# Optimization experiments

Hardware: AMD Instinct MI355X
Metric: run time of the kernel (lower is better)

The kernel has to match this reference:

```python
import jax, jax.numpy as jnp
import numpy as np

# Static config (Swin-T stage 1, SW-MSA)
B = 32; H = 56; W = 56; C = 96; NH = 3; WS = 7; SHIFT = 3
N = WS * WS                 # tokens per window (49)
NW = (H // WS) * (W // WS)  # windows per image (64)
HD = C // NH                # head dim (32)
SCALE = HD ** -0.5
EPS = 1e-3  # keras LayerNormalization default epsilon


def _rel_index():
    # Matches tf.stack(tf.meshgrid(h, w)) with default 'xy' indexing
    xx, yy = np.meshgrid(np.arange(WS), np.arange(WS))
    coords = np.stack([xx, yy]).reshape(2, -1)              # [2, 49]
    rel = (coords[:, :, None] - coords[:, None, :]).transpose(1, 2, 0)
    rel[:, :, 0] += WS - 1
    rel[:, :, 1] += WS - 1
    rel[:, :, 0] *= 2 * WS - 1
    return rel.sum(-1)                                       # [49, 49]

REL_IDX = jnp.asarray(_rel_index())


def _attn_mask():
    # Standard Swin shifted-window attention mask
    img = np.zeros((H, W))
    cnt = 0
    sl = (slice(0, -WS), slice(-WS, -SHIFT), slice(-SHIFT, None))
    for hs in sl:
        for ws_ in sl:
            img[hs, ws_] = cnt
            cnt += 1
    win = img.reshape(H // WS, WS, W // WS, WS).transpose(0, 2, 1, 3).reshape(-1, N)
    diff = win[:, None, :] - win[:, :, None]
    return jnp.asarray(np.where(diff != 0, -100.0, 0.0), dtype=np.float32)  # [nW,49,49]

MASK = _attn_mask()


def _ln(x, g, b):
    mu = x.mean(-1, keepdims=True)
    var = ((x - mu) ** 2).mean(-1, keepdims=True)
    return (x - mu) / jnp.sqrt(var + EPS) * g + b


def setup_inputs() -> dict:
    key = jax.random.key(0)
    ks = jax.random.split(key, 6)
    f32 = jnp.float32
    return {
        "x": jax.random.normal(ks[0], (B, H * W, C), f32),
        "norm1_g": jnp.ones((C,), f32), "norm1_b": jnp.zeros((C,), f32),
        "qkv_w": jax.random.normal(ks[1], (C, 3 * C), f32) * 0.02,
        "qkv_b": jnp.zeros((3 * C,), f32),
        "bias_table": jax.random.normal(ks[2], ((2 * WS - 1) ** 2, NH), f32) * 0.02,
        "proj_w": jax.random.normal(ks[3], (C, C), f32) * 0.02,
        "proj_b": jnp.zeros((C,), f32),
        "norm2_g": jnp.ones((C,), f32), "norm2_b": jnp.zeros((C,), f32),
        "fc1_w": jax.random.normal(ks[4], (C, 4 * C), f32) * 0.02,
        "fc1_b": jnp.zeros((4 * C,), f32),
        "fc2_w": jax.random.normal(ks[5], (4 * C, C), f32) * 0.02,
        "fc2_b": jnp.zeros((C,), f32),
    }


def reference(x, norm1_g, norm1_b, qkv_w, qkv_b, bias_table, proj_w, proj_b,
              norm2_g, norm2_b, fc1_w, fc1_b, fc2_w, fc2_b):
    shortcut = x
    h = _ln(x, norm1_g, norm1_b).reshape(B, H, W, C)
    # cyclic shift (SW-MSA)
    h = jnp.roll(h, (-SHIFT, -SHIFT), axis=(1, 2))
    # window partition -> [B*nW, N, C]
    h = h.reshape(B, H // WS, WS, W // WS, WS, C).transpose(0, 1, 3, 2, 4, 5).reshape(-1, N, C)
    qkv = (h @ qkv_w + qkv_b).reshape(-1, N, 3, NH, HD).transpose(2, 0, 3, 1, 4)
    q, k, v = qkv[0], qkv[1], qkv[2]            # each [B*nW, NH, N, HD]
    attn = jnp.einsum('bhnd,bhmd->bhnm', q * SCALE, k)
    bias = bias_table[REL_IDX.reshape(-1)].reshape(N, N, NH).transpose(2, 0, 1)
    attn = attn + bias[None]
    attn = attn.reshape(B, NW, NH, N, N) + MASK[None, :, None]
    attn = attn.reshape(-1, NH, N, N)
    # NOTE: source applies softmax twice (once in branch, once unconditionally)
    attn = jax.nn.softmax(jax.nn.softmax(attn, axis=-1), axis=-1)
    o = jnp.einsum('bhnm,bhmd->bhnd', attn, v).transpose(0, 2, 1, 3).reshape(-1, N, C)
    o = o @ proj_w + proj_b
    # window reverse + reverse cyclic shift
    o = o.reshape(B, H // WS, W // WS, WS, WS, C).transpose(0, 1, 3, 2, 4, 5).reshape(B, H, W, C)
    o = jnp.roll(o, (SHIFT, SHIFT), axis=(1, 2)).reshape(B, H * W, C)
    x = shortcut + o
    y = _ln(x, norm2_g, norm2_b)
    # NOTE: source Mlp applies gelu in Dense activation AND again in call -> double gelu
    y = jax.nn.gelu(y @ fc1_w + fc1_b, approximate=False)
    y = jax.nn.gelu(y, approximate=False)
    y = y @ fc2_w + fc2_b
    return x + y
```

## Files before the change

### kernel.cpp

```cpp
#include <hip/hip_runtime.h>
#include <math.h>

#define BB   32
#define HH   56
#define WWI  56
#define CC   96
#define NHD  3
#define WSZ  7
#define SHF  3
#define NTK  49
#define NWIN 64
#define HDM  32
#define TOT  (BB*HH*WWI)
#define QKSCALE 0.17677669529663687f
#define LEPS 1e-3f

typedef __attribute__((ext_vector_type(8))) short s8v;
typedef __attribute__((ext_vector_type(4))) float fx4;
typedef unsigned long long ull_t;

#define MFMA16(a,b,c) __builtin_amdgcn_mfma_f32_16x16x32_bf16((a),(b),(c),0,0,0)

__device__ __forceinline__ unsigned short f2bf(float f) {
    union { float f; unsigned u; } v; v.f = f;
    unsigned r = v.u + 0x7FFFu + ((v.u >> 16) & 1u);
    return (unsigned short)(r >> 16);
}

__device__ __forceinline__ float gelu_t(float x) {
    float x3 = x * x * x;
    float z = -1.5957691216f * fmaf(0.044715f, x3, x);
    return x * __builtin_amdgcn_rcpf(1.f + __expf(z));
}

__device__ __forceinline__ int wtok_to_orig(int wt) {
    int win = wt / NTK;
    int p   = wt - win * NTK;
    int b   = win >> 6;
    int w   = win & 63;
    int wi = w >> 3, wj = w & 7;
    int pi = p / WSZ, pj = p - pi * WSZ;
    int r = wi * WSZ + pi + SHF; if (r >= HH) r -= HH;
    int c = wj * WSZ + pj + SHF; if (c >= WWI) c -= WWI;
    return b * (HH * WWI) + r * WWI + c;
}

__device__ __forceinline__ void ln_frag(const float* __restrict__ row,
                                        const float* __restrict__ gg,
                                        const float* __restrict__ bb,
                                        int g4, s8v ha[3])
{
    float h[24];
    #pragma unroll
    for (int ks = 0; ks < 3; ++ks) {
        fx4 v0 = *reinterpret_cast<const fx4*>(row + ks * 32 + g4 * 8);
        fx4 v1 = *reinterpret_cast<const fx4*>(row + ks * 32 + g4 * 8 + 4);
        h[ks*8+0]=v0.x; h[ks*8+1]=v0.y; h[ks*8+2]=v0.z; h[ks*8+3]=v0.w;
        h[ks*8+4]=v1.x; h[ks*8+5]=v1.y; h[ks*8+6]=v1.z; h[ks*8+7]=v1.w;
    }
    float s = 0.f, s2 = 0.f;
    #pragma unroll
    for (int j = 0; j < 24; ++j) { s += h[j]; s2 = fmaf(h[j], h[j], s2); }
    s  += __shfl_xor(s, 16);  s  += __shfl_xor(s, 32);
    s2 += __shfl_xor(s2, 16); s2 += __shfl_xor(s2, 32);
    const float mu = s * (1.f/CC);
    const float rs = rsqrtf(s2 * (1.f/CC) - mu * mu + LEPS);
    #pragma unroll
    for (int ks = 0; ks < 3; ++ks) {
        union { s8v v; unsigned short u[8]; } p;
        #pragma unroll
        for (int j = 0; j < 8; ++j) {
            int c = ks * 32 + g4 * 8 + j;
            p.u[j] = f2bf((h[ks*8+j] - mu) * rs * gg[c] + bb[c]);
        }
        ha[ks] = p.v;
    }
}

extern "C" __global__ void p0_prep(const float* __restrict__ qw, const float* __restrict__ pw,
                                   const float* __restrict__ w1, const float* __restrict__ w2,
                                   const float* __restrict__ btab,
                                   unsigned short* __restrict__ wsw)
{
    int i = blockIdx.x * 256 + threadIdx.x;
    if (i < 27648) {
        int n = i / 96, k = i - n * 96;
        float v = qw[k * 288 + n];
        if (n < 96) v *= QKSCALE;
        wsw[i] = f2bf(v);
    } else if (i < 36864) {
        int j = i - 27648; int n = j / 96, k = j - n * 96;
        wsw[i] = f2bf(pw[k * 96 + n]);
    } else if (i < 73728) {
        int j = i - 36864; int n = j / 96, k = j - n * 96;
        wsw[i] = f2bf(w1[k * 384 + n]);
    } else if (i < 110592) {
        int j = i - 73728; int n = j / 384, k = j - n * 384;
        wsw[i] = f2bf(w2[k * 96 + n]);
    } else if (i < 148224) {
        float* bm = (float*)(wsw + 110592);
        int j = i - 110592;
        int n = j & 63, mh = j >> 6;
        int m = mh % 49, t = mh / 49;
        int hd = t % 3, cls = t / 3;
        float val = 0.f;
        if (n < 49) {
            int it = m / 7, jt = m - it * 7;
            int iu = n / 7, ju = n - iu * 7;
            int li  = (cls & 2) ? (it < 4 ? 1 : 2) : 0;
            int lj  = (cls & 1) ? (jt < 4 ? 1 : 2) : 0;
            int lui = (cls & 2) ? (iu < 4 ? 1 : 2) : 0;
            int luj = (cls & 1) ? (ju < 4 ? 1 : 2) : 0;
            int bidx = (jt - ju + 6) * 13 + (it - iu + 6);
            val = btab[bidx * 3 + hd] + ((li*3+lj) == (lui*3+luj) ? 0.f : -100.f);
        }
        bm[j] = val;
    }
}

#define LDH 104
extern "C" __global__ void __launch_bounds__(512, 4) k1_qkv(
    const float* __restrict__ x, const float* __restrict__ g1, const float* __restrict__ b1,
    const unsigned short* __restrict__ qwt, const float* __restrict__ qb,
    unsigned short* __restrict__ qkvb)
{
    __shared__ unsigned short Wc[96 * LDH];
    const int tid = threadIdx.x, wave = tid >> 6, lane = tid & 63;
    const int l15 = lane & 15, g4 = lane >> 4;
    const int blk = blockIdx.x;

    s8v ha[3];
    {
        const int orig = wtok_to_orig(blk * 128 + wave * 16 + l15);
        ln_frag(x + (size_t)orig * CC, g1, b1, g4, ha);
    }

    for (int ck = 0; ck < 3; ++ck) {
        for (int i = tid; i < 96 * 12; i += 512) {
            int r = i / 12, k0 = (i - r * 12) * 8;
            *reinterpret_cast<s8v*>(&Wc[r * LDH + k0]) =
                *reinterpret_cast<const s8v*>(&qwt[(ck * 96 + r) * 96 + k0]);
        }
        __syncthreads();
        fx4 acc[6];
        #pragma unroll
        for (int nt = 0; nt < 6; ++nt) acc[nt] = (fx4){0.f,0.f,0.f,0.f};
        #pragma unroll
        for (int ks = 0; ks < 3; ++ks) {
            #pragma unroll
            for (int nt = 0; nt < 6; ++nt) {
                s8v b = *reinterpret_cast<const s8v*>(&Wc[(nt*16 + l15)*LDH + ks*32 + g4*8]);
                acc[nt] = MFMA16(ha[ks], b, acc[nt]);
            }
        }
        const int rowb = blk * 128 + wave * 16 + g4 * 4;
        const float qmul = (ck == 0) ? QKSCALE : 1.f;
        #pragma unroll
        for (int nt = 0; nt < 6; ++nt) {
            const int col = ck * 96 + nt * 16 + l15;
            const float qbc = qb[col] * qmul;
            #pragma unroll
            for (int r = 0; r < 4; ++r)
                qkvb[(size_t)(rowb + r) * 288 + col] = f2bf(acc[nt][r] + qbc);
        }
        __syncthreads();
    }
}

extern "C" __global__ void __launch_bounds__(64, 2) k2_attn(
    unsigned short* __restrict__ qkvb, const float* __restrict__ bm)
{
    __shared__ unsigned short P[64][72];
    const int lane = threadIdx.x;
    const int l15 = lane & 15, g4 = lane >> 4;
    const int task = blockIdx.x;
    const int win = task / 3, h = task - win * 3;
    const int g0  = win * NTK;
    const int w   = win & 63;
    const int cls = (((w >> 3) == 7) ? 2 : 0) + (((w & 7) == 7) ? 1 : 0);
    const float* BMh = bm + ((size_t)(cls * 3 + h)) * 49 * 64;

    s8v aq[4], bk[4];
    #pragma unroll
    for (int mt = 0; mt < 4; ++mt) {
        int tok = mt * 16 + l15; if (tok > 48) tok = 48;
        const unsigned short* qp = &qkvb[(size_t)(g0 + tok) * 288 + h * HDM + g4 * 8];
        aq[mt] = *reinterpret_cast<const s8v*>(qp);
        bk[mt] = *reinterpret_cast<const s8v*>(qp + 96);
    }

    fx4 sc[4][4];
    #pragma unroll
    for (int mt = 0; mt < 4; ++mt)
        #pragma unroll
        for (int nt = 0; nt < 4; ++nt)
            sc[mt][nt] = MFMA16(aq[mt], bk[nt], ((fx4){0.f,0.f,0.f,0.f}));

    #pragma unroll
    for (int mt = 0; mt < 4; ++mt) {
        #pragma unroll
        for (int r = 0; r < 4; ++r) {
            const int m = mt * 16 + g4 * 4 + r;
            const int mc = m > 48 ? 48 : m;
            float rs1 = 0.f;
            #pragma unroll
            for (int nt = 0; nt < 4; ++nt) {
                const int n = nt * 16 + l15;
                float s = sc[mt][nt][r] + BMh[mc * 64 + n];
                float e = (n < NTK) ? __expf(s) : 0.f;
                sc[mt][nt][r] = e;
                rs1 += e;
            }
            rs1 += __shfl_xor(rs1, 1); rs1 += __shfl_xor(rs1, 2);
            rs1 += __shfl_xor(rs1, 4); rs1 += __shfl_xor(rs1, 8);
            const float iv1 = 1.f / rs1;
            float rs2 = 0.f;
            #pragma unroll
            for (int nt = 0; nt < 4; ++nt) {
                const int n = nt * 16 + l15;
                float e2 = (n < NTK) ? __expf(sc[mt][nt][r] * iv1) : 0.f;
                sc[mt][nt][r] = e2;
                rs2 += e2;
            }
            rs2 += __shfl_xor(rs2, 1); rs2 += __shfl_xor(rs2, 2);
            rs2 += __shfl_xor(rs2, 4); rs2 += __shfl_xor(rs2, 8);
            const float iv2 = 1.f / rs2;
            #pragma unroll
            for (int nt = 0; nt < 4; ++nt)
                P[m][nt * 16 + l15] = f2bf(sc[mt][nt][r] * iv2);
        }
    }
    __syncthreads();

    fx4 oc[4][2];
    #pragma unroll
    for (int mt = 0; mt < 4; ++mt) { oc[mt][0] = (fx4){0.f,0.f,0.f,0.f}; oc[mt][1] = (fx4){0.f,0.f,0.f,0.f}; }
    #pragma unroll
    for (int ks = 0; ks < 2; ++ks) {
        s8v vb[2];
        #pragma unroll
        for (int nt = 0; nt < 2; ++nt) {
            union { s8v v; unsigned short u[8]; } pv;
            #pragma unroll
            for (int j = 0; j < 8; ++j) {
                int tok = ks * 32 + g4 * 8 + j; if (tok > 48) tok = 48;
                pv.u[j] = qkvb[(size_t)(g0 + tok) * 288 + 192 + h * HDM + nt * 16 + l15];
            }
            vb[nt] = pv.v;
        }
        #pragma unroll
        for (int mt = 0; mt < 4; ++mt) {
            s8v pa = *reinterpret_cast<const s8v*>(&P[mt * 16 + l15][ks * 32 + g4 * 8]);
            oc[mt][0] = MFMA16(pa, vb[0], oc[mt][0]);
            oc[mt][1] = MFMA16(pa, vb[1], oc[mt][1]);
        }
    }
    #pragma unroll
    for (int mt = 0; mt < 4; ++mt) {
        #pragma unroll
        for (int r = 0; r < 4; ++r) {
            const int m = mt * 16 + g4 * 4 + r;
            if (m < NTK) {
                qkvb[(size_t)(g0 + m) * 288 + h * HDM + l15]      = f2bf(oc[mt][0][r]);
                qkvb[(size_t)(g0 + m) * 288 + h * HDM + 16 + l15] = f2bf(oc[mt][1][r]);
            }
        }
    }
}

extern "C" __global__ void __launch_bounds__(512, 4) k2b_proj(
    const unsigned short* __restrict__ qkvb, const unsigned short* __restrict__ pwt,
    const float* __restrict__ pb, const float* __restrict__ x, float* __restrict__ out)
{
    __shared__ unsigned short Wc[96 * LDH];
    const int tid = threadIdx.x, wave = tid >> 6, lane = tid & 63;
    const int l15 = lane & 15, g4 = lane >> 4;
    const int blk = blockIdx.x;

    for (int i = tid; i < 96 * 12; i += 512) {
        int r = i / 12, k0 = (i - r * 12) * 8;
        *reinterpret_cast<s8v*>(&Wc[r * LDH + k0]) =
            *reinterpret_cast<const s8v*>(&pwt[r * 96 + k0]);
    }
    const unsigned short* arow = qkvb + (size_t)(blk * 128 + wave * 16 + l15) * 288 + g4 * 8;
    s8v a0 = *reinterpret_cast<const s8v*>(arow);
    s8v a1 = *reinterpret_cast<const s8v*>(arow + 32);
    s8v a2 = *reinterpret_cast<const s8v*>(arow + 64);
    __syncthreads();

    fx4 acc[6];
    #pragma unroll
    for (int nt = 0; nt < 6; ++nt) acc[nt] = (fx4){0.f,0.f,0.f,0.f};
    #pragma unroll
    for (int nt = 0; nt < 6; ++nt) {
        acc[nt] = MFMA16(a0, *reinterpret_cast<const s8v*>(&Wc[(nt*16 + l15)*LDH +  0 + g4*8]), acc[nt]);
        acc[nt] = MFMA16(a1, *reinterpret_cast<const s8v*>(&Wc[(nt*16 + l15)*LDH + 32 + g4*8]), acc[nt]);
        acc[nt] = MFMA16(a2, *reinterpret_cast<const s8v*>(&Wc[(nt*16 + l15)*LDH + 64 + g4*8]), acc[nt]);
    }
    int orig[4];
    #pragma unroll
    for (int r = 0; r < 4; ++r)
        orig[r] = wtok_to_orig(blk * 128 + wave * 16 + g4 * 4 + r);
    #pragma unroll
    for (int nt = 0; nt < 6; ++nt) {
        const int col = nt * 16 + l15;
        const float pbc = pb[col];
        #pragma unroll
        for (int r = 0; r < 4; ++r) {
            const size_t idx = (size_t)orig[r] * CC + col;
            out[idx] = acc[nt][r] + pbc + x[idx];
        }
    }
}

#define LDA 72
#define K3_LD(ck_, idx_, dst_) { \
    if ((idx_) < 768) { int r_ = (idx_) / 12, k0_ = ((idx_) - r_ * 12) * 8; \
        dst_ = *reinterpret_cast<const s8v*>(&w1t[((ck_) * 64 + r_) * 96 + k0_]); } \
    else { int j_ = (idx_) - 768; int r_ = j_ >> 3, k0_ = (j_ & 7) * 8; \
        dst_ = *reinterpret_cast<const s8v*>(&w2t[r_ * 384 + (ck_) * 64 + k0_]); } }
#define K3_ST(idx_, src_) { \
    if ((idx_) < 768) { int r_ = (idx_) / 12, k0_ = ((idx_) - r_ * 12) * 8; \
        *reinterpret_cast<s8v*>(&W1c[r_ * LDH + k0_]) = src_; } \
    else { int j_ = (idx_) - 768; int r_ = j_ >> 3, k0_ = (j_ & 7) * 8; \
        *reinterpret_cast<s8v*>(&W2c[r_ * LDA + k0_]) = src_; } }

extern "C" __global__ void __launch_bounds__(512, 4) k3_mlp(
    float* __restrict__ xio, const float* __restrict__ g2, const float* __restrict__ b2,
    const unsigned short* __restrict__ w1t, const float* __restrict__ bf1,
    const unsigned short* __restrict__ w2t, const float* __restrict__ bf2)
{
    __shared__ unsigned short W1c[64 * LDH];
    __shared__ unsigned short Ac[128 * LDA];
    __shared__ unsigned short W2c[96 * LDA];
    const int tid = threadIdx.x, wave = tid >> 6, lane = tid & 63;
    const int l15 = lane & 15, g4 = lane >> 4;
    const int blk = blockIdx.x;

    s8v ha[3];
    ln_frag(xio + (size_t)(blk * 128 + wave * 16 + l15) * CC, g2, b2, g4, ha);

    {
        s8v v0, v1, v2;
        K3_LD(0, tid, v0); K3_LD(0, tid + 512, v1); K3_LD(0, tid + 1024, v2);
        K3_ST(tid, v0); K3_ST(tid + 512, v1); K3_ST(tid + 1024, v2);
    }
    __syncthreads();

    fx4 oacc[6];
    #pragma unroll
    for (int nt = 0; nt < 6; ++nt) oacc[nt] = (fx4){0.f,0.f,0.f,0.f};

    for (int ck = 0; ck < 6; ++ck) {
        s8v n0, n1, n2;
        if (ck < 5) { K3_LD(ck + 1, tid, n0); K3_LD(ck + 1, tid + 512, n1); K3_LD(ck + 1, tid + 1024, n2); }

        fx4 a1[4];
        #pragma unroll
        for (int nt = 0; nt < 4; ++nt) a1[nt] = (fx4){0.f,0.f,0.f,0.f};
        #pragma unroll
        for (int ks = 0; ks < 3; ++ks) {
            #pragma unroll
            for (int nt = 0; nt < 4; ++nt) {
                s8v b = *reinterpret_cast<const s8v*>(&W1c[(nt*16 + l15)*LDH + ks*32 + g4*8]);
                a1[nt] = MFMA16(ha[ks], b, a1[nt]);
            }
        }
        #pragma unroll
        for (int nt = 0; nt < 4; ++nt) {
            const float bb = bf1[ck * 64 + nt * 16 + l15];
            #pragma unroll
            for (int r = 0; r < 4; ++r) {
                float v0 = a1[nt][r] + bb;
                Ac[(wave*16 + g4*4 + r) * LDA + nt*16 + l15] = f2bf(gelu_t(gelu_t(v0)));
            }
        }
        #pragma unroll
        for (int ks = 0; ks < 2; ++ks) {
            s8v a = *reinterpret_cast<const s8v*>(&Ac[(wave*16 + l15)*LDA + ks*32 + g4*8]);
            #pragma unroll
            for (int nt = 0; nt < 6; ++nt) {
                s8v b = *reinterpret_cast<const s8v*>(&W2c[(nt*16 + l15)*LDA + ks*32 + g4*8]);
                oacc[nt] = MFMA16(a, b, oacc[nt]);
            }
        }
        __syncthreads();
        if (ck < 5) {
            K3_ST(tid, n0); K3_ST(tid + 512, n1); K3_ST(tid + 1024, n2);
            __syncthreads();
        }
    }

    const int rowb = blk * 128 + wave * 16 + g4 * 4;
    #pragma unroll
    for (int nt = 0; nt < 6; ++nt) {
        const int col = nt * 16 + l15;
        const float bb = bf2[col];
        #pragma unroll
        for (int r = 0; r < 4; ++r) {
            const size_t idx = (size_t)(rowb + r) * CC + col;
            xio[idx] = xio[idx] + oacc[nt][r] + bb;
        }
    }
}

extern "C" void kernel_launch(void* const* d_in, const int* in_sizes, int n_in,
                              void* d_out, int out_size, void* d_ws, size_t ws_size,
                              hipStream_t stream)
{
    const float* x    = (const float*)d_in[0];
    const float* n1g  = (const float*)d_in[1];
    const float* n1b  = (const float*)d_in[2];
    const float* qw   = (const float*)d_in[3];
    const float* qb   = (const float*)d_in[4];
    const float* btab = (const float*)d_in[5];
    const float* pw   = (const float*)d_in[6];
    const float* pb   = (const float*)d_in[7];
    const float* n2g  = (const float*)d_in[8];
    const float* n2b  = (const float*)d_in[9];
    const float* w1   = (const float*)d_in[10];
    const float* bf1  = (const float*)d_in[11];
    const float* w2   = (const float*)d_in[12];
    const float* bf2  = (const float*)d_in[13];
    float* out = (float*)d_out;

    unsigned short* qkvb = (unsigned short*)d_ws;
    unsigned short* wbf = qkvb + (size_t)TOT * 288;
    unsigned short* qwt = wbf;
    unsigned short* pwt = qwt + 288 * 96;
    unsigned short* w1t = pwt + 96 * 96;
    unsigned short* w2t = w1t + 384 * 96;
    float* bmt = (float*)(wbf + 110592);

    p0_prep <<<579, 256, 0, stream>>>(qw, pw, w1, w2, btab, wbf);
    k1_qkv  <<<TOT/128, 512, 0, stream>>>(x, n1g, n1b, qwt, qb, qkvb);
    k2_attn <<<BB*NWIN*NHD, 64, 0, stream>>>(qkvb, bmt);
    k2b_proj<<<TOT/128, 512, 0, stream>>>(qkvb, pwt, pb, x, out);
    k3_mlp  <<<TOT/128, 512, 0, stream>>>(out, n2g, n2b, w1t, bf1, w2t, bf2);
}
```

Baseline: 146.4 us.

## Pre-swizzle MLP weights into MFMA fragment order and read them directly from global

The prep kernel now stores fc1 and fc2 weights in per-lane MFMA B-fragment order, so the MLP kernel loads each fragment with one coalesced 16-byte global read. This removes staging the weights through LDS and the block-wide barriers around it. Blocks shrink to 256 threads covering 64 rows, which lowers LDS use and changes occupancy. The cost is that every wave re-reads the full weight set from L2/L1 instead of sharing one LDS copy.

```diff
diff --git a/kernel.cpp b/kernel.cpp
--- a/kernel.cpp
+++ b/kernel.cpp
@@ -92,10 +92,22 @@
         int j = i - 27648; int n = j / 96, k = j - n * 96;
         wsw[i] = f2bf(pw[k * 96 + n]);
     } else if (i < 73728) {
-        int j = i - 36864; int n = j / 96, k = j - n * 96;
+        int j = i - 36864;
+        int e = j & 7, f = j >> 3;
+        int lane = f & 63, fid = f >> 6;
+        int ks = fid % 3, t = fid / 3;
+        int nt = t & 3, ck = t >> 2;
+        int n = ck * 64 + nt * 16 + (lane & 15);
+        int k = ks * 32 + (lane >> 4) * 8 + e;
         wsw[i] = f2bf(w1[k * 384 + n]);
     } else if (i < 110592) {
-        int j = i - 73728; int n = j / 384, k = j - n * 384;
+        int j = i - 73728;
+        int e = j & 7, f = j >> 3;
+        int lane = f & 63, fid = f >> 6;
+        int ks = fid & 1, t = fid >> 1;
+        int nt = t % 6, ck = t / 6;
+        int n = nt * 16 + (lane & 15);
+        int k = ck * 64 + ks * 32 + (lane >> 4) * 8 + e;
         wsw[i] = f2bf(w2[k * 96 + n]);
     } else if (i < 148224) {
         float* bm = (float*)(wsw + 110592);
@@ -314,47 +326,24 @@
 }
 
 #define LDA 72
-#define K3_LD(ck_, idx_, dst_) { \
-    if ((idx_) < 768) { int r_ = (idx_) / 12, k0_ = ((idx_) - r_ * 12) * 8; \
-        dst_ = *reinterpret_cast<const s8v*>(&w1t[((ck_) * 64 + r_) * 96 + k0_]); } \
-    else { int j_ = (idx_) - 768; int r_ = j_ >> 3, k0_ = (j_ & 7) * 8; \
-        dst_ = *reinterpret_cast<const s8v*>(&w2t[r_ * 384 + (ck_) * 64 + k0_]); } }
-#define K3_ST(idx_, src_) { \
-    if ((idx_) < 768) { int r_ = (idx_) / 12, k0_ = ((idx_) - r_ * 12) * 8; \
-        *reinterpret_cast<s8v*>(&W1c[r_ * LDH + k0_]) = src_; } \
-    else { int j_ = (idx_) - 768; int r_ = j_ >> 3, k0_ = (j_ & 7) * 8; \
-        *reinterpret_cast<s8v*>(&W2c[r_ * LDA + k0_]) = src_; } }
-
-extern "C" __global__ void __launch_bounds__(512, 4) k3_mlp(
+extern "C" __global__ void __launch_bounds__(256, 3) k3_mlp(
     float* __restrict__ xio, const float* __restrict__ g2, const float* __restrict__ b2,
-    const unsigned short* __restrict__ w1t, const float* __restrict__ bf1,
-    const unsigned short* __restrict__ w2t, const float* __restrict__ bf2)
-{
-    __shared__ unsigned short W1c[64 * LDH];
-    __shared__ unsigned short Ac[128 * LDA];
-    __shared__ unsigned short W2c[96 * LDA];
+    const unsigned short* __restrict__ w1f, const float* __restrict__ bf1,
+    const unsigned short* __restrict__ w2f, const float* __restrict__ bf2)
+{
+    __shared__ unsigned short Ac[64 * LDA];
     const int tid = threadIdx.x, wave = tid >> 6, lane = tid & 63;
     const int l15 = lane & 15, g4 = lane >> 4;
-    const int blk = blockIdx.x;
+    const int row0 = blockIdx.x * 64 + wave * 16;
 
     s8v ha[3];
-    ln_frag(xio + (size_t)(blk * 128 + wave * 16 + l15) * CC, g2, b2, g4, ha);
-
-    {
-        s8v v0, v1, v2;
-        K3_LD(0, tid, v0); K3_LD(0, tid + 512, v1); K3_LD(0, tid + 1024, v2);
-        K3_ST(tid, v0); K3_ST(tid + 512, v1); K3_ST(tid + 1024, v2);
-    }
-    __syncthreads();
+    ln_frag(xio + (size_t)(row0 + l15) * CC, g2, b2, g4, ha);
 
     fx4 oacc[6];
     #pragma unroll
     for (int nt = 0; nt < 6; ++nt) oacc[nt] = (fx4){0.f,0.f,0.f,0.f};
 
     for (int ck = 0; ck < 6; ++ck) {
-        s8v n0, n1, n2;
-        if (ck < 5) { K3_LD(ck + 1, tid, n0); K3_LD(ck + 1, tid + 512, n1); K3_LD(ck + 1, tid + 1024, n2); }
-
         fx4 a1[4];
         #pragma unroll
         for (int nt = 0; nt < 4; ++nt) a1[nt] = (fx4){0.f,0.f,0.f,0.f};
@@ -362,7 +351,8 @@
         for (int ks = 0; ks < 3; ++ks) {
             #pragma unroll
             for (int nt = 0; nt < 4; ++nt) {
-                s8v b = *reinterpret_cast<const s8v*>(&W1c[(nt*16 + l15)*LDH + ks*32 + g4*8]);
+                s8v b = *reinterpret_cast<const s8v*>(
+                    &w1f[(((ck * 4 + nt) * 3 + ks) * 64 + lane) * 8]);
                 a1[nt] = MFMA16(ha[ks], b, a1[nt]);
             }
         }
@@ -380,18 +370,14 @@
             s8v a = *reinterpret_cast<const s8v*>(&Ac[(wave*16 + l15)*LDA + ks*32 + g4*8]);
             #pragma unroll
             for (int nt = 0; nt < 6; ++nt) {
-                s8v b = *reinterpret_cast<const s8v*>(&W2c[(nt*16 + l15)*LDA + ks*32 + g4*8]);
+                s8v b = *reinterpret_cast<const s8v*>(
+                    &w2f[(((ck * 6 + nt) * 2 + ks) * 64 + lane) * 8]);
                 oacc[nt] = MFMA16(a, b, oacc[nt]);
             }
         }
-        __syncthreads();
-        if (ck < 5) {
-            K3_ST(tid, n0); K3_ST(tid + 512, n1); K3_ST(tid + 1024, n2);
-            __syncthreads();
-        }
-    }
-
-    const int rowb = blk * 128 + wave * 16 + g4 * 4;
+    }
+
+    const int rowb = row0 + g4 * 4;
     #pragma unroll
     for (int nt = 0; nt < 6; ++nt) {
         const int col = nt * 16 + l15;
@@ -427,14 +413,14 @@
     unsigned short* qkvb = (unsigned short*)d_ws;
     unsigned short* wbf = qkvb + (size_t)TOT * 288;
     unsigned short* qwt = wbf;
-    unsigned short* pwt = qwt + 288 * 96;
-    unsigned short* w1t = pwt + 96 * 96;
-    unsigned short* w2t = w1t + 384 * 96;
+    unsigned short* pwt = qwt + 27648;
+    unsigned short* w1f = pwt + 9216;
+    unsigned short* w2f = w1f + 36864;
     float* bmt = (float*)(wbf + 110592);
 
     p0_prep <<<579, 256, 0, stream>>>(qw, pw, w1, w2, btab, wbf);
     k1_qkv  <<<TOT/128, 512, 0, stream>>>(x, n1g, n1b, qwt, qb, qkvb);
     k2_attn <<<BB*NWIN*NHD, 64, 0, stream>>>(qkvb, bmt);
     k2b_proj<<<TOT/128, 512, 0, stream>>>(qkvb, pwt, pb, x, out);
-    k3_mlp  <<<TOT/128, 512, 0, stream>>>(out, n2g, n2b, w1t, bf1, w2t, bf2);
-}
+    k3_mlp  <<<TOT/64, 256, 0, stream>>>(out, n2g, n2b, w1f, bf1, w2f, bf2);
+}
```

Result: faster. 141.3 us (-3.5%).
